# Kernel tuning notes

Measured on AMD Instinct MI355X. Metric: run time of the kernel, lower is better.

## Reference

```python
import jax, jax.numpy as jnp
import numpy as np

# Vim-S config
B, L, D, DEPTH = 16, 197, 384, 24
DI, DS, DTR = 768, 16, 24  # d_inner=2*D, d_state, dt_rank=ceil(D/16)
NUM_CLASSES = 1000
EPS = 1e-5


def setup_inputs() -> dict:
    key = jax.random.key(0)
    ks = jax.random.split(key, 12)
    f = jnp.float32
    rn = lambda k, shp, s=0.02: jax.random.normal(k, shp, f) * s
    inp = {
        'x': jax.random.normal(ks[0], (B, 3, 224, 224), f),
        'patch_w': rn(ks[1], (D, 3, 16, 16)),
        'patch_b': jnp.zeros((D,), f),
        'cls_token': rn(ks[2], (1, 1, D)),
        'pos_embed': rn(ks[3], (1, L, D)),
        'in_proj_w': rn(ks[4], (DEPTH, 2 * DI, D)),
        'conv_w': rn(ks[5], (DEPTH, DI, 1, 4), 0.1),  # depthwise causal conv, d_conv=4
        'conv_b': jnp.zeros((DEPTH, DI), f),
        'x_proj_w': rn(ks[6], (DEPTH, DTR + 2 * DS, DI)),
        'dt_proj_w': rn(ks[7], (DEPTH, DI, DTR), 0.1),
        'dt_proj_b': jnp.full((DEPTH, DI), float(np.log(np.expm1(0.01))), f),
        'A_log': jnp.log(jnp.broadcast_to(jnp.arange(1, DS + 1, dtype=f), (DEPTH, DI, DS))),
        'D_ssm': jnp.ones((DEPTH, DI), f),
        'out_proj_w': rn(ks[8], (DEPTH, D, DI)),
        'norm_w': jnp.ones((DEPTH, D), f),
        'norm_b': jnp.zeros((DEPTH, D), f),
        'normf_w': jnp.ones((D,), f),
        'normf_b': jnp.zeros((D,), f),
        'head_w': rn(ks[9], (NUM_CLASSES, D)),
        'head_b': jnp.zeros((NUM_CLASSES,), f),
    }
    return inp


def _ln(u, w, b):
    mu = u.mean(-1, keepdims=True)
    v = ((u - mu) ** 2).mean(-1, keepdims=True)
    return (u - mu) * jax.lax.rsqrt(v + EPS) * w + b


def _silu(u):
    return u * jax.nn.sigmoid(u)


def _mixer(u, Win, Wc, bc, Wx, Wdt, bdt, Alog, Dp, Wout):
    # u: [B, L, D]
    xz = jnp.einsum('bld,ed->ble', u, Win)            # [B, L, 2*DI]
    xc, z = jnp.split(xz, 2, axis=-1)
    # causal depthwise conv1d (d_conv=4): pad 3 on the left
    xt = jnp.pad(xc.transpose(0, 2, 1), ((0, 0), (0, 0), (3, 0)))
    xt = jax.lax.conv_general_dilated(xt, Wc, (1,), 'VALID',
                                      dimension_numbers=('NCH', 'OIH', 'NCH'),
                                      feature_group_count=DI)
    xc = _silu((xt + bc[None, :, None]).transpose(0, 2, 1))  # [B, L, DI]
    dbl = jnp.einsum('bld,ed->ble', xc, Wx)           # [B, L, DTR+2*DS]
    dt = jax.nn.softplus(jnp.einsum('blr,dr->bld', dbl[..., :DTR], Wdt) + bdt)
    Bm = dbl[..., DTR:DTR + DS]                       # [B, L, DS]
    Cm = dbl[..., DTR + DS:]                          # [B, L, DS]
    A = -jnp.exp(Alog)                                # [DI, DS]
    dA = jnp.exp(jnp.einsum('bld,dn->bldn', dt, A))   # [B, L, DI, DS]
    dBx = jnp.einsum('bld,bln->bldn', dt * xc, Bm)    # [B, L, DI, DS]

    def step(h, inps):
        dA_t, dBx_t, C_t = inps
        h = dA_t * h + dBx_t                          # [B, DI, DS]
        return h, jnp.einsum('bdn,bn->bd', h, C_t)

    h0 = jnp.zeros((u.shape[0], DI, DS), u.dtype)
    _, ys = jax.lax.scan(step, h0, (dA.transpose(1, 0, 2, 3),
                                    dBx.transpose(1, 0, 2, 3),
                                    Cm.transpose(1, 0, 2)))
    y = ys.transpose(1, 0, 2) + xc * Dp               # [B, L, DI]
    y = y * _silu(z)
    return jnp.einsum('ble,de->bld', y, Wout)         # [B, L, D]


def reference(x, patch_w, patch_b, cls_token, pos_embed, in_proj_w, conv_w, conv_b,
              x_proj_w, dt_proj_w, dt_proj_b, A_log, D_ssm, out_proj_w,
              norm_w, norm_b, normf_w, normf_b, head_w, head_b):
    b = x.shape[0]
    # patch embed: Conv2d(3, D, 16, stride 16)
    feat = jax.lax.conv_general_dilated(x, patch_w, (16, 16), 'VALID',
                                        dimension_numbers=('NCHW', 'OIHW', 'NCHW'))
    feat = feat + patch_b[None, :, None, None]
    tokens = feat.reshape(b, D, -1).transpose(0, 2, 1)          # [B, 196, D]
    h = jnp.concatenate([jnp.broadcast_to(cls_token, (b, 1, D)), tokens], axis=1)
    h = h + pos_embed                                           # [B, 197, D]

    def layer(carry, p):
        hid, res = carry
        Win, Wc, bc, Wx, Wdt, bdt, Alog, Dp, Wout, nw, nb = p
        res = res + hid                # (hidden + residual), first layer: residual = hidden
        hid = _mixer(_ln(res, nw, nb), Win, Wc, bc, Wx, Wdt, bdt, Alog, Dp, Wout)
        return (hid, res), None

    (hid, res), _ = jax.lax.scan(layer, (h, jnp.zeros_like(h)),
                                 (in_proj_w, conv_w, conv_b, x_proj_w, dt_proj_w,
                                  dt_proj_b, A_log, D_ssm, out_proj_w, norm_w, norm_b))
    out = _ln(res + hid, normf_w, normf_b)
    return out[:, 0] @ head_w.T + head_b                        # [B, num_classes]
```

## Files before the change

kernel.cpp:

```cpp
#include <hip/hip_runtime.h>
#include <hip/hip_bf16.h>
#include <math.h>

#define BB     16
#define LL     197
#define DD     384
#define DEPTH  24
#define DI     768
#define DSN    16
#define DTR    24
#define NC     1000
#define TT     (BB*LL)
#define NPATCH 196
#define EPSV   1e-5f

#define NCHUNK 12
#define CH     17

typedef __attribute__((ext_vector_type(8))) short short8;
typedef __attribute__((ext_vector_type(4))) short short4v;
typedef __attribute__((ext_vector_type(4))) float f32x4;

__device__ __forceinline__ short f2bf(float f) {
  union { float f; unsigned u; } v; v.f = f;
  unsigned u = v.u + 0x7fffu + ((v.u >> 16) & 1u);
  return (short)(u >> 16);
}

__device__ __forceinline__ void gload16(const short* g, const short* l) {
  __builtin_amdgcn_global_load_lds(
      (const __attribute__((address_space(1))) unsigned int*)g,
      (__attribute__((address_space(3))) unsigned int*)l, 16, 0, 0);
}

__global__ __launch_bounds__(256) void k_cvt(const float* __restrict__ src,
                                             short* __restrict__ dst, int n) {
  int i = (blockIdx.x * 256 + threadIdx.x) * 4;
  if (i + 3 < n) {
    float4 v = *(const float4*)&src[i];
    short4v o = {f2bf(v.x), f2bf(v.y), f2bf(v.z), f2bf(v.w)};
    *(short4v*)&dst[i] = o;
  } else {
    for (int j = 0; i + j < n && j < 4; j++) dst[i + j] = f2bf(src[i + j]);
  }
}

__global__ __launch_bounds__(256) void k_init(const float* __restrict__ cls,
                                              const float* __restrict__ pos,
                                              float* __restrict__ res,
                                              float* __restrict__ hid) {
  int i = blockIdx.x * 256 + threadIdx.x;
  if (i < TT * DD) res[i] = 0.f;
  if (i < BB * DD) {
    int b = i / DD, d = i % DD;
    hid[(size_t)(b * LL) * DD + d] = cls[d] + pos[d];
  }
}

__global__ __launch_bounds__(256) void k_patch(const float* __restrict__ x,
                                               const float* __restrict__ pw,
                                               const float* __restrict__ pb,
                                               const float* __restrict__ pos,
                                               float* __restrict__ hid) {
  __shared__ short sA[64 * 40];
  __shared__ short sB[64 * 40];
  const int tid = threadIdx.x;
  const int m0 = blockIdx.x * 64, n0 = blockIdx.y * 64;
  const int srow = tid >> 2;
  const int skq = (tid & 3) * 8;
  const int lane = tid & 63, w = tid >> 6;
  const int wm = (w >> 1) * 32, wn = (w & 1) * 32;
  const int fr = lane & 15;
  const int fk = (lane >> 4) * 8;
  f32x4 acc[2][2] = {};
  const int m = m0 + srow;
  const int b = m / NPATCH;
  const int p = m % NPATCH;
  const int ph = p / 14, pwi = p % 14;
  const float* Wrow = pw + (size_t)(n0 + srow) * 768 + skq;
  for (int k0 = 0; k0 < 768; k0 += 32) {
    int k = k0 + skq;
    int c = k >> 8, rr = (k >> 4) & 15, kw = k & 15;
    const float* xrow = &x[(size_t)(((b * 3 + c) * 224) + (ph * 16 + rr)) * 224 +
                           (pwi * 16 + kw)];
    float4 a0 = *(const float4*)&xrow[0];
    float4 a1 = *(const float4*)&xrow[4];
    float4 b0 = *(const float4*)&Wrow[k0];
    float4 b1 = *(const float4*)&Wrow[k0 + 4];
    short8 av = {f2bf(a0.x), f2bf(a0.y), f2bf(a0.z), f2bf(a0.w),
                 f2bf(a1.x), f2bf(a1.y), f2bf(a1.z), f2bf(a1.w)};
    short8 bv = {f2bf(b0.x), f2bf(b0.y), f2bf(b0.z), f2bf(b0.w),
                 f2bf(b1.x), f2bf(b1.y), f2bf(b1.z), f2bf(b1.w)};
    *(short8*)&sA[srow * 40 + skq] = av;
    *(short8*)&sB[srow * 40 + skq] = bv;
    __syncthreads();
    short8 af0 = *(const short8*)&sA[(wm + fr) * 40 + fk];
    short8 af1 = *(const short8*)&sA[(wm + 16 + fr) * 40 + fk];
    short8 bf0 = *(const short8*)&sB[(wn + fr) * 40 + fk];
    short8 bf1 = *(const short8*)&sB[(wn + 16 + fr) * 40 + fk];
    acc[0][0] = __builtin_amdgcn_mfma_f32_16x16x32_bf16(af0, bf0, acc[0][0], 0, 0, 0);
    acc[0][1] = __builtin_amdgcn_mfma_f32_16x16x32_bf16(af0, bf1, acc[0][1], 0, 0, 0);
    acc[1][0] = __builtin_amdgcn_mfma_f32_16x16x32_bf16(af1, bf0, acc[1][0], 0, 0, 0);
    acc[1][1] = __builtin_amdgcn_mfma_f32_16x16x32_bf16(af1, bf1, acc[1][1], 0, 0, 0);
    __syncthreads();
  }
#pragma unroll
  for (int i = 0; i < 2; i++)
#pragma unroll
    for (int j = 0; j < 2; j++)
#pragma unroll
      for (int q = 0; q < 4; q++) {
        int mm = m0 + wm + i * 16 + (lane >> 4) * 4 + q;
        int nn = n0 + wn + j * 16 + (lane & 15);
        int b2 = mm / NPATCH, pp = mm % NPATCH;
        int tok = b2 * LL + 1 + pp;
        hid[(size_t)tok * DD + nn] = acc[i][j][q] + pb[nn] + pos[(size_t)(1 + pp) * DD + nn];
      }
}

__global__ __launch_bounds__(256) void k_gemm128(const short* __restrict__ A, int lda,
                                                 const short* __restrict__ W, int ldb,
                                                 float* __restrict__ C, int ldc,
                                                 int M, int N, int K) {
  __shared__ short sA[128 * 32];
  __shared__ short sB[128 * 32];
  const int tid = threadIdx.x;
  const int lane = tid & 63, w = tid >> 6;
  const int m0 = blockIdx.x * 128, n0 = blockIdx.y * 128;
  const int wm = (w >> 1) * 64, wn = (w & 1) * 64;
  const int fr = lane & 15;
  const int fk = (lane >> 4) * 8;
  const int q0 = w * 2, q1 = w * 2 + 1;
  const int sr0 = q0 * 16 + (lane >> 2);
  const int sr1 = q1 * 16 + (lane >> 2);
  const int scol = (lane & 3) * 8;
  f32x4 acc[4][4] = {};
  const short* Ab0 = A + (size_t)(m0 + sr0) * lda + scol;
  const short* Ab1 = A + (size_t)(m0 + sr1) * lda + scol;
  const short* Bb0 = W + (size_t)(n0 + sr0) * ldb + scol;
  const short* Bb1 = W + (size_t)(n0 + sr1) * ldb + scol;
  for (int k0 = 0; k0 < K; k0 += 32) {
    gload16(Ab0 + k0, &sA[q0 * 512]);
    gload16(Ab1 + k0, &sA[q1 * 512]);
    gload16(Bb0 + k0, &sB[q0 * 512]);
    gload16(Bb1 + k0, &sB[q1 * 512]);
    __syncthreads();
    short8 af[4], bf[4];
#pragma unroll
    for (int i = 0; i < 4; i++) {
      af[i] = *(const short8*)&sA[(wm + i * 16 + fr) * 32 + fk];
      bf[i] = *(const short8*)&sB[(wn + i * 16 + fr) * 32 + fk];
    }
#pragma unroll
    for (int i = 0; i < 4; i++)
#pragma unroll
      for (int j = 0; j < 4; j++)
        acc[i][j] = __builtin_amdgcn_mfma_f32_16x16x32_bf16(af[i], bf[j], acc[i][j], 0, 0, 0);
    __syncthreads();
  }
#pragma unroll
  for (int i = 0; i < 4; i++)
#pragma unroll
    for (int j = 0; j < 4; j++)
#pragma unroll
      for (int q = 0; q < 4; q++) {
        int mm = m0 + wm + i * 16 + (lane >> 4) * 4 + q;
        int nn = n0 + wn + j * 16 + fr;
        if (mm < M) C[(size_t)mm * ldc + nn] = acc[i][j][q];
      }
}

__global__ __launch_bounds__(256) void k_gemm64(const short* __restrict__ A, int lda,
                                                const short* __restrict__ W, int ldb,
                                                float* __restrict__ C, int ldc,
                                                int M, int N, int K) {
  __shared__ short sA[64 * 32];
  __shared__ short sB[64 * 32];
  const int tid = threadIdx.x;
  const int lane = tid & 63, w = tid >> 6;
  const int m0 = blockIdx.x * 64, n0 = blockIdx.y * 64;
  const int wm = (w >> 1) * 32, wn = (w & 1) * 32;
  const int fr = lane & 15;
  const int fk = (lane >> 4) * 8;
  const int srow = w * 16 + (lane >> 2);
  const int scol = (lane & 3) * 8;
  f32x4 acc[2][2] = {};
  const short* Ab = A + (size_t)(m0 + srow) * lda + scol;
  const short* Bb = W + (size_t)(n0 + srow) * ldb + scol;
  for (int k0 = 0; k0 < K; k0 += 32) {
    gload16(Ab + k0, &sA[w * 512]);
    gload16(Bb + k0, &sB[w * 512]);
    __syncthreads();
    short8 af0 = *(const short8*)&sA[(wm + fr) * 32 + fk];
    short8 af1 = *(const short8*)&sA[(wm + 16 + fr) * 32 + fk];
    short8 bf0 = *(const short8*)&sB[(wn + fr) * 32 + fk];
    short8 bf1 = *(const short8*)&sB[(wn + 16 + fr) * 32 + fk];
    acc[0][0] = __builtin_amdgcn_mfma_f32_16x16x32_bf16(af0, bf0, acc[0][0], 0, 0, 0);
    acc[0][1] = __builtin_amdgcn_mfma_f32_16x16x32_bf16(af0, bf1, acc[0][1], 0, 0, 0);
    acc[1][0] = __builtin_amdgcn_mfma_f32_16x16x32_bf16(af1, bf0, acc[1][0], 0, 0, 0);
    acc[1][1] = __builtin_amdgcn_mfma_f32_16x16x32_bf16(af1, bf1, acc[1][1], 0, 0, 0);
    __syncthreads();
  }
#pragma unroll
  for (int i = 0; i < 2; i++)
#pragma unroll
    for (int j = 0; j < 2; j++)
#pragma unroll
      for (int q = 0; q < 4; q++) {
        int mm = m0 + wm + i * 16 + (lane >> 4) * 4 + q;
        int nn = n0 + wn + j * 16 + fr;
        if (mm < M) C[(size_t)mm * ldc + nn] = acc[i][j][q];
      }
}

__global__ __launch_bounds__(256) void k_conv(const float* __restrict__ xz,
                                              const float* __restrict__ wc,
                                              const float* __restrict__ bc,
                                              float* __restrict__ xc,
                                              short* __restrict__ xcbf) {
  int i = blockIdx.x * 256 + threadIdx.x;
  if (i >= TT * (DI / 4)) return;
  int eg = i % (DI / 4);
  int t = i / (DI / 4);
  int e = eg * 4;
  int b = t / LL, l = t % LL;
  const float* base = xz + (size_t)(b * LL) * (2 * DI) + e;
  float4 w0 = *(const float4*)&wc[(e + 0) * 4];
  float4 w1 = *(const float4*)&wc[(e + 1) * 4];
  float4 w2 = *(const float4*)&wc[(e + 2) * 4];
  float4 w3 = *(const float4*)&wc[(e + 3) * 4];
  float4 acc = *(const float4*)&bc[e];
  if (l >= 3) {
    float4 xv = *(const float4*)&base[(size_t)(l - 3) * (2 * DI)];
    acc.x += xv.x * w0.x; acc.y += xv.y * w1.x; acc.z += xv.z * w2.x; acc.w += xv.w * w3.x;
  }
  if (l >= 2) {
    float4 xv = *(const float4*)&base[(size_t)(l - 2) * (2 * DI)];
    acc.x += xv.x * w0.y; acc.y += xv.y * w1.y; acc.z += xv.z * w2.y; acc.w += xv.w * w3.y;
  }
  if (l >= 1) {
    float4 xv = *(const float4*)&base[(size_t)(l - 1) * (2 * DI)];
    acc.x += xv.x * w0.z; acc.y += xv.y * w1.z; acc.z += xv.z * w2.z; acc.w += xv.w * w3.z;
  }
  {
    float4 xv = *(const float4*)&base[(size_t)l * (2 * DI)];
    acc.x += xv.x * w0.w; acc.y += xv.y * w1.w; acc.z += xv.z * w2.w; acc.w += xv.w * w3.w;
  }
  acc.x = acc.x / (1.f + __expf(-acc.x));
  acc.y = acc.y / (1.f + __expf(-acc.y));
  acc.z = acc.z / (1.f + __expf(-acc.z));
  acc.w = acc.w / (1.f + __expf(-acc.w));
  *(float4*)&xc[(size_t)t * DI + e] = acc;
  short4v ov = {f2bf(acc.x), f2bf(acc.y), f2bf(acc.z), f2bf(acc.w)};
  *(short4v*)&xcbf[(size_t)t * DI + e] = ov;
}

__global__ __launch_bounds__(256) void k_xd(const short* __restrict__ xcbf,
                                            const short* __restrict__ wx,
                                            const short* __restrict__ wdt,
                                            const float* __restrict__ dbias,
                                            float* __restrict__ dbl,
                                            float* __restrict__ dtb) {
  __shared__ short sDT[16 * 40];
  const int tid = threadIdx.x;
  const int t0 = blockIdx.x * 16;
  const int lane = tid & 63, w = tid >> 6;
  const int fr = lane & 15;
  const int fk = (lane >> 4) * 8;
  f32x4 accx = {};
  const short* Arow = xcbf + (size_t)(t0 + fr) * DI + fk;
  const short* Wrow = wx + (size_t)(w * 16 + fr) * DI + fk;
#pragma unroll
  for (int k0 = 0; k0 < DI; k0 += 32) {
    short8 af = *(const short8*)&Arow[k0];
    short8 bf = *(const short8*)&Wrow[k0];
    accx = __builtin_amdgcn_mfma_f32_16x16x32_bf16(af, bf, accx, 0, 0, 0);
  }
  {
    int nn = w * 16 + fr;
#pragma unroll
    for (int q = 0; q < 4; q++) {
      int row = (lane >> 4) * 4 + q;
      int t = t0 + row;
      if (nn >= DTR && nn < 56) dbl[(size_t)t * 56 + nn] = accx[q];
      if (w < 2) sDT[row * 40 + nn] = (nn < DTR) ? f2bf(accx[q]) : (short)0;
    }
  }
  __syncthreads();
  short8 adt = *(const short8*)&sDT[fr * 40 + fk];
  const int g = lane >> 4;
#pragma unroll
  for (int jj = 0; jj < 12; jj++) {
    int j = w * 12 + jj;
    short8 bdt = short8{0, 0, 0, 0, 0, 0, 0, 0};
    if (g < 3) bdt = *(const short8*)&wdt[(size_t)(j * 16 + fr) * DTR + g * 8];
    f32x4 p = {};
    p = __builtin_amdgcn_mfma_f32_16x16x32_bf16(adt, bdt, p, 0, 0, 0);
    int nc = j * 16 + fr;
    float bv = dbias[nc];
#pragma unroll
    for (int q = 0; q < 4; q++) {
      int t = t0 + (lane >> 4) * 4 + q;
      float v = p[q] + bv;
      v = (v > 20.f) ? v : __logf(1.f + __expf(v));
      dtb[(size_t)t * DI + nc] = v;
    }
  }
}

__global__ __launch_bounds__(256) void k_scan1(const float* __restrict__ dt,
                                               const float* __restrict__ xc,
                                               const float* __restrict__ dbl,
                                               const float* __restrict__ Alog,
                                               float* __restrict__ Aprod,
                                               float* __restrict__ Hend) {
  const int tid = threadIdx.x;
  const int e = blockIdx.x * 128 + (tid >> 1);
  const int nh = tid & 1;
  const int b = blockIdx.y;
  const int c = blockIdx.z;
  float4 al0 = *(const float4*)&Alog[(size_t)e * DSN + nh * 8];
  float4 al1 = *(const float4*)&Alog[(size_t)e * DSN + nh * 8 + 4];
  float negA[8] = {-__expf(al0.x), -__expf(al0.y), -__expf(al0.z), -__expf(al0.w),
                   -__expf(al1.x), -__expf(al1.y), -__expf(al1.z), -__expf(al1.w)};
  float h[8] = {};
  float asum = 0.f;
  const int l0 = c * CH;
  const int l1 = (l0 + CH < LL) ? (l0 + CH) : LL;
  const size_t tbase = (size_t)b * LL;
  for (int l = l0; l < l1; l++) {
    size_t t = tbase + l;
    float dtv = dt[t * DI + e];
    float xcv = xc[t * DI + e];
    float4 B0 = *(const float4*)&dbl[t * 56 + DTR + nh * 8];
    float4 B1 = *(const float4*)&dbl[t * 56 + DTR + nh * 8 + 4];
    float dx = dtv * xcv;
    float Bv[8] = {B0.x, B0.y, B0.z, B0.w, B1.x, B1.y, B1.z, B1.w};
#pragma unroll
    for (int j = 0; j < 8; j++)
      h[j] = __expf(dtv * negA[j]) * h[j] + dx * Bv[j];
    asum += dtv;
  }
  size_t ci = (((size_t)c * BB + b) * DI + e) * DSN + nh * 8;
  *(float4*)&Aprod[ci] = float4{__expf(asum * negA[0]), __expf(asum * negA[1]),
                                __expf(asum * negA[2]), __expf(asum * negA[3])};
  *(float4*)&Aprod[ci + 4] = float4{__expf(asum * negA[4]), __expf(asum * negA[5]),
                                    __expf(asum * negA[6]), __expf(asum * negA[7])};
  *(float4*)&Hend[ci] = float4{h[0], h[1], h[2], h[3]};
  *(float4*)&Hend[ci + 4] = float4{h[4], h[5], h[6], h[7]};
}

__global__ __launch_bounds__(256) void k_scan2(const float* __restrict__ dt,
                                               const float* __restrict__ xc,
                                               const float* __restrict__ xz,
                                               const float* __restrict__ dbl,
                                               const float* __restrict__ Alog,
                                               const float* __restrict__ Dp,
                                               const float* __restrict__ Aprod,
                                               const float* __restrict__ Hend,
                                               short* __restrict__ ybf) {
  const int tid = threadIdx.x;
  const int e = blockIdx.x * 128 + (tid >> 1);
  const int nh = tid & 1;
  const int b = blockIdx.y;
  const int c = blockIdx.z;
  float4 al0 = *(const float4*)&Alog[(size_t)e * DSN + nh * 8];
  float4 al1 = *(const float4*)&Alog[(size_t)e * DSN + nh * 8 + 4];
  float negA[8] = {-__expf(al0.x), -__expf(al0.y), -__expf(al0.z), -__expf(al0.w),
                   -__expf(al1.x), -__expf(al1.y), -__expf(al1.z), -__expf(al1.w)};
  const float dpv = Dp[e];
  float h[8] = {};
  const size_t cstride = (size_t)BB * DI * DSN;
  const size_t cbase = (((size_t)b * DI + e) * DSN) + nh * 8;
  for (int cp = 0; cp < c; cp++) {
    size_t ci = (size_t)cp * cstride + cbase;
    float4 a0 = *(const float4*)&Aprod[ci];
    float4 a1 = *(const float4*)&Aprod[ci + 4];
    float4 e0 = *(const float4*)&Hend[ci];
    float4 e1 = *(const float4*)&Hend[ci + 4];
    h[0] = a0.x * h[0] + e0.x; h[1] = a0.y * h[1] + e0.y;
    h[2] = a0.z * h[2] + e0.z; h[3] = a0.w * h[3] + e0.w;
    h[4] = a1.x * h[4] + e1.x; h[5] = a1.y * h[5] + e1.y;
    h[6] = a1.z * h[6] + e1.z; h[7] = a1.w * h[7] + e1.w;
  }
  const int l0 = c * CH;
  const int l1 = (l0 + CH < LL) ? (l0 + CH) : LL;
  const size_t tbase = (size_t)b * LL;
  for (int l = l0; l < l1; l++) {
    size_t t = tbase + l;
    float dtv = dt[t * DI + e];
    float xcv = xc[t * DI + e];
    float zv = xz[t * (2 * DI) + DI + e];
    float4 B0 = *(const float4*)&dbl[t * 56 + DTR + nh * 8];
    float4 B1 = *(const float4*)&dbl[t * 56 + DTR + nh * 8 + 4];
    float4 C0 = *(const float4*)&dbl[t * 56 + DTR + DSN + nh * 8];
    float4 C1 = *(const float4*)&dbl[t * 56 + DTR + DSN + nh * 8 + 4];
    float dx = dtv * xcv;
    float Bv[8] = {B0.x, B0.y, B0.z, B0.w, B1.x, B1.y, B1.z, B1.w};
    float Cv[8] = {C0.x, C0.y, C0.z, C0.w, C1.x, C1.y, C1.z, C1.w};
    float acc = 0.f;
#pragma unroll
    for (int j = 0; j < 8; j++) {
      h[j] = __expf(dtv * negA[j]) * h[j] + dx * Bv[j];
      acc += h[j] * Cv[j];
    }
    acc += __shfl_xor(acc, 1);
    if (nh == 0) {
      float sz = zv * (1.f / (1.f + __expf(-zv)));
      ybf[t * DI + e] = f2bf((acc + xcv * dpv) * sz);
    }
  }
}

__global__ __launch_bounds__(256) void k_addln(float* __restrict__ res,
                                               const float* __restrict__ hid,
                                               short* __restrict__ u,
                                               const float* __restrict__ nw,
                                               const float* __restrict__ nb) {
  const int lane = threadIdx.x & 63;
  const int t = blockIdx.x * 4 + (threadIdx.x >> 6);
  float r[6];
  float s = 0.f, sq = 0.f;
#pragma unroll
  for (int j = 0; j < 6; j++) {
    int d = lane + j * 64;
    float v = res[(size_t)t * DD + d] + hid[(size_t)t * DD + d];
    res[(size_t)t * DD + d] = v;
    r[j] = v;
    s += v; sq += v * v;
  }
#pragma unroll
  for (int o = 32; o > 0; o >>= 1) { s += __shfl_xor(s, o); sq += __shfl_xor(sq, o); }
  float mu = s * (1.f / 384.f);
  float var = sq * (1.f / 384.f) - mu * mu;
  float rs = rsqrtf(var + EPSV);
#pragma unroll
  for (int j = 0; j < 6; j++) {
    int d = lane + j * 64;
    u[(size_t)t * DD + d] = f2bf((r[j] - mu) * rs * nw[d] + nb[d]);
  }
}

__global__ __launch_bounds__(256) void k_final(const float* __restrict__ res,
                                               const float* __restrict__ hid,
                                               const float* __restrict__ nfw,
                                               const float* __restrict__ nfb,
                                               const float* __restrict__ hw,
                                               const float* __restrict__ hb,
                                               float* __restrict__ out) {
  const int b = blockIdx.y;
  const int c0 = blockIdx.x * 125;
  const int tid = threadIdx.x;
  __shared__ float u0[DD];
  __shared__ float ls[4], lq[4];
  const size_t t0 = (size_t)b * LL * DD;
  float v0 = res[t0 + tid] + hid[t0 + tid];
  float v1 = (tid < 128) ? (res[t0 + 256 + tid] + hid[t0 + 256 + tid]) : 0.f;
  float s = v0 + v1, sq = v0 * v0 + v1 * v1;
#pragma unroll
  for (int o = 32; o > 0; o >>= 1) { s += __shfl_xor(s, o); sq += __shfl_xor(sq, o); }
  if ((tid & 63) == 0) { ls[tid >> 6] = s; lq[tid >> 6] = sq; }
  __syncthreads();
  float st = ls[0] + ls[1] + ls[2] + ls[3];
  float qt = lq[0] + lq[1] + lq[2] + lq[3];
  float mu = st * (1.f / 384.f);
  float var = qt * (1.f / 384.f) - mu * mu;
  float rs = rsqrtf(var + EPSV);
  u0[tid] = (v0 - mu) * rs * nfw[tid] + nfb[tid];
  if (tid < 128) u0[256 + tid] = (v1 - mu) * rs * nfw[256 + tid] + nfb[256 + tid];
  __syncthreads();
  int c = c0 + tid;
  if (tid < 125 && c < NC) {
    float acc = hb[c];
    const float* wrow = hw + (size_t)c * DD;
    for (int d = 0; d < DD; d += 4) {
      float4 w4 = *(const float4*)&wrow[d];
      acc += u0[d] * w4.x + u0[d + 1] * w4.y + u0[d + 2] * w4.z + u0[d + 3] * w4.w;
    }
    out[(size_t)b * NC + c] = acc;
  }
}

extern "C" void kernel_launch(void* const* d_in, const int* in_sizes, int n_in,
                              void* d_out, int out_size, void* d_ws, size_t ws_size,
                              hipStream_t stream) {
  const float* x       = (const float*)d_in[0];
  const float* patch_w = (const float*)d_in[1];
  const float* patch_b = (const float*)d_in[2];
  const float* cls     = (const float*)d_in[3];
  const float* pos     = (const float*)d_in[4];
  const float* in_proj = (const float*)d_in[5];
  const float* conv_w  = (const float*)d_in[6];
  const float* conv_b  = (const float*)d_in[7];
  const float* x_proj  = (const float*)d_in[8];
  const float* dt_w    = (const float*)d_in[9];
  const float* dt_b    = (const float*)d_in[10];
  const float* A_log   = (const float*)d_in[11];
  const float* D_ssm   = (const float*)d_in[12];
  const float* out_w   = (const float*)d_in[13];
  const float* norm_w  = (const float*)d_in[14];
  const float* norm_b  = (const float*)d_in[15];
  const float* normf_w = (const float*)d_in[16];
  const float* normf_b = (const float*)d_in[17];
  const float* head_w  = (const float*)d_in[18];
  const float* head_b  = (const float*)d_in[19];
  float* out = (float*)d_out;

  float* ws = (float*)d_ws;
  float* res = ws;  ws += (size_t)TT * DD;
  float* hid = ws;  ws += (size_t)TT * DD;
  float* u_r = ws;  ws += (size_t)TT * DD;
  float* xzb = ws;  ws += (size_t)TT * 2 * DI;
  float* xcb = ws;  ws += (size_t)TT * DI;
  float* dbl = ws;  ws += (size_t)TT * 56;
  float* dtb = ws;  ws += (size_t)TT * DI;
  float* ybf_r = ws; ws += (size_t)TT * DI / 2;
  float* xcbf_r = ws; ws += (size_t)TT * DI / 2;
  float* Aprod = ws; ws += (size_t)NCHUNK * BB * DI * DSN;
  float* Hend  = ws; ws += (size_t)NCHUNK * BB * DI * DSN;
  short* winbf  = (short*)ws; ws += (size_t)DEPTH * 2 * DI * DD / 2;
  short* woutbf = (short*)ws; ws += (size_t)DEPTH * DD * DI / 2;
  short* wxbf   = (short*)ws; ws += (size_t)DEPTH * 56 * DI / 2;
  short* wdtbf  = (short*)ws; ws += (size_t)DEPTH * DI * DTR / 2;

  short* u    = (short*)u_r;
  short* ybf  = (short*)ybf_r;
  short* xcbf = (short*)xcbf_r;

  {
    int n1 = DEPTH * 2 * DI * DD;
    k_cvt<<<(n1 / 4 + 255) / 256, 256, 0, stream>>>(in_proj, winbf, n1);
    int n2 = DEPTH * DD * DI;
    k_cvt<<<(n2 / 4 + 255) / 256, 256, 0, stream>>>(out_w, woutbf, n2);
    int n3 = DEPTH * 56 * DI;
    k_cvt<<<(n3 / 4 + 255) / 256, 256, 0, stream>>>(x_proj, wxbf, n3);
    int n4 = DEPTH * DI * DTR;
    k_cvt<<<(n4 / 4 + 255) / 256, 256, 0, stream>>>(dt_w, wdtbf, n4);
  }

  k_init<<<(TT * DD + 255) / 256, 256, 0, stream>>>(cls, pos, res, hid);
  k_patch<<<dim3(49, 6), 256, 0, stream>>>(x, patch_w, patch_b, pos, hid);

  for (int layer = 0; layer < DEPTH; layer++) {
    k_addln<<<TT / 4, 256, 0, stream>>>(res, hid, u, norm_w + layer * DD,
                                        norm_b + layer * DD);
    k_gemm128<<<dim3(25, 12), 256, 0, stream>>>(
        u, DD, winbf + (size_t)layer * 2 * DI * DD, DD, xzb, 2 * DI, TT, 2 * DI, DD);
    k_conv<<<(TT * (DI / 4) + 255) / 256, 256, 0, stream>>>(
        xzb, conv_w + layer * DI * 4, conv_b + layer * DI, xcb, xcbf);
    k_xd<<<dim3(TT / 16), 256, 0, stream>>>(
        xcbf, wxbf + (size_t)layer * 56 * DI, wdtbf + (size_t)layer * DI * DTR,
        dt_b + layer * DI, dbl, dtb);
    k_scan1<<<dim3(DI / 128, BB, NCHUNK - 1), 256, 0, stream>>>(
        dtb, xcb, dbl, A_log + (size_t)layer * DI * DSN, Aprod, Hend);
    k_scan2<<<dim3(DI / 128, BB, NCHUNK), 256, 0, stream>>>(
        dtb, xcb, xzb, dbl, A_log + (size_t)layer * DI * DSN,
        D_ssm + layer * DI, Aprod, Hend, ybf);
    k_gemm64<<<dim3(50, 6), 256, 0, stream>>>(
        ybf, DI, woutbf + (size_t)layer * DD * DI, DI, hid, DD, TT, DD, DI);
  }

  k_final<<<dim3(8, BB), 256, 0, stream>>>(res, hid, normf_w, normf_b, head_w, head_b, out);
}
```

Measured before the change: 2.594 ms.

## Fuse layernorm into in_proj GEMM, conv into x_proj, residual into out_proj

Removes the separate add+layernorm kernel. The in_proj GEMM now computes row statistics itself and normalizes fp32 residual rows into bf16 LDS tiles on the fly. The depthwise conv+SiLU is merged into the x_proj/dt kernel through shared memory, which drops the bf16 xc buffer. out_proj now accumulates directly into the residual (+=), which removes the hid buffer, and the four weight conversions are batched into one launch. This saves launches and global round-trips, but each in_proj block re-reads its residual rows for statistics, and the A-tile path loses async global-to-LDS loads.

```diff
diff --git a/kernel.cpp b/kernel.cpp
--- a/kernel.cpp
+++ b/kernel.cpp
@@ -33,9 +33,18 @@
       (__attribute__((address_space(3))) unsigned int*)l, 16, 0, 0);
 }
 
-__global__ __launch_bounds__(256) void k_cvt(const float* __restrict__ src,
-                                             short* __restrict__ dst, int n) {
-  int i = (blockIdx.x * 256 + threadIdx.x) * 4;
+__global__ __launch_bounds__(256) void k_cvt4(const float* __restrict__ s0, short* __restrict__ d0, int n0,
+                                              const float* __restrict__ s1, short* __restrict__ d1, int n1,
+                                              const float* __restrict__ s2, short* __restrict__ d2, int n2,
+                                              const float* __restrict__ s3, short* __restrict__ d3, int n3,
+                                              int b0, int b1, int b2) {
+  int blk = blockIdx.x;
+  const float* src; short* dst; int n; int lb;
+  if (blk < b0)      { src = s0; dst = d0; n = n0; lb = blk; }
+  else if (blk < b1) { src = s1; dst = d1; n = n1; lb = blk - b0; }
+  else if (blk < b2) { src = s2; dst = d2; n = n2; lb = blk - b1; }
+  else               { src = s3; dst = d3; n = n3; lb = blk - b2; }
+  int i = (lb * 256 + threadIdx.x) * 4;
   if (i + 3 < n) {
     float4 v = *(const float4*)&src[i];
     short4v o = {f2bf(v.x), f2bf(v.y), f2bf(v.z), f2bf(v.w)};
@@ -47,13 +56,11 @@
 
 __global__ __launch_bounds__(256) void k_init(const float* __restrict__ cls,
                                               const float* __restrict__ pos,
-                                              float* __restrict__ res,
-                                              float* __restrict__ hid) {
+                                              float* __restrict__ res) {
   int i = blockIdx.x * 256 + threadIdx.x;
-  if (i < TT * DD) res[i] = 0.f;
   if (i < BB * DD) {
     int b = i / DD, d = i % DD;
-    hid[(size_t)(b * LL) * DD + d] = cls[d] + pos[d];
+    res[(size_t)(b * LL) * DD + d] = cls[d] + pos[d];
   }
 }
 
@@ -61,7 +68,7 @@
                                                const float* __restrict__ pw,
                                                const float* __restrict__ pb,
                                                const float* __restrict__ pos,
-                                               float* __restrict__ hid) {
+                                               float* __restrict__ res) {
   __shared__ short sA[64 * 40];
   __shared__ short sB[64 * 40];
   const int tid = threadIdx.x;
@@ -114,19 +121,42 @@
         int nn = n0 + wn + j * 16 + (lane & 15);
         int b2 = mm / NPATCH, pp = mm % NPATCH;
         int tok = b2 * LL + 1 + pp;
-        hid[(size_t)tok * DD + nn] = acc[i][j][q] + pb[nn] + pos[(size_t)(1 + pp) * DD + nn];
+        res[(size_t)tok * DD + nn] = acc[i][j][q] + pb[nn] + pos[(size_t)(1 + pp) * DD + nn];
       }
 }
 
-__global__ __launch_bounds__(256) void k_gemm128(const short* __restrict__ A, int lda,
-                                                 const short* __restrict__ W, int ldb,
-                                                 float* __restrict__ C, int ldc,
-                                                 int M, int N, int K) {
+__global__ __launch_bounds__(256) void k_lngemm(const float* __restrict__ R,
+                                                const float* __restrict__ nw,
+                                                const float* __restrict__ nb,
+                                                const short* __restrict__ W,
+                                                float* __restrict__ C) {
   __shared__ short sA[128 * 32];
   __shared__ short sB[128 * 32];
+  __shared__ float smu[128], srs[128];
+  __shared__ float snw[DD], snb[DD];
   const int tid = threadIdx.x;
   const int lane = tid & 63, w = tid >> 6;
   const int m0 = blockIdx.x * 128, n0 = blockIdx.y * 128;
+  if (tid < 96) *(float4*)&snw[tid * 4] = *(const float4*)&nw[tid * 4];
+  else if (tid < 192) *(float4*)&snb[(tid - 96) * 4] = *(const float4*)&nb[(tid - 96) * 4];
+  {
+    int r = tid >> 1, hf = tid & 1;
+    const float* row = R + (size_t)(m0 + r) * DD + hf * 192;
+    float s = 0.f, sq = 0.f;
+#pragma unroll 4
+    for (int j = 0; j < 48; j++) {
+      float4 v = *(const float4*)&row[j * 4];
+      s += v.x + v.y + v.z + v.w;
+      sq += v.x * v.x + v.y * v.y + v.z * v.z + v.w * v.w;
+    }
+    s += __shfl_xor(s, 1); sq += __shfl_xor(sq, 1);
+    if (hf == 0) {
+      float mu = s * (1.f / 384.f);
+      float var = sq * (1.f / 384.f) - mu * mu;
+      smu[r] = mu; srs[r] = rsqrtf(var + EPSV);
+    }
+  }
+  __syncthreads();
   const int wm = (w >> 1) * 64, wn = (w & 1) * 64;
   const int fr = lane & 15;
   const int fk = (lane >> 4) * 8;
@@ -135,15 +165,41 @@
   const int sr1 = q1 * 16 + (lane >> 2);
   const int scol = (lane & 3) * 8;
   f32x4 acc[4][4] = {};
-  const short* Ab0 = A + (size_t)(m0 + sr0) * lda + scol;
-  const short* Ab1 = A + (size_t)(m0 + sr1) * lda + scol;
-  const short* Bb0 = W + (size_t)(n0 + sr0) * ldb + scol;
-  const short* Bb1 = W + (size_t)(n0 + sr1) * ldb + scol;
-  for (int k0 = 0; k0 < K; k0 += 32) {
-    gload16(Ab0 + k0, &sA[q0 * 512]);
-    gload16(Ab1 + k0, &sA[q1 * 512]);
+  const short* Bb0 = W + (size_t)(n0 + sr0) * DD + scol;
+  const short* Bb1 = W + (size_t)(n0 + sr1) * DD + scol;
+  const float* Ar0 = R + (size_t)(m0 + sr0) * DD + scol;
+  const float* Ar1 = R + (size_t)(m0 + sr1) * DD + scol;
+  const float mu0 = smu[sr0], rs0 = srs[sr0];
+  const float mu1 = smu[sr1], rs1 = srs[sr1];
+  for (int k0 = 0; k0 < DD; k0 += 32) {
     gload16(Bb0 + k0, &sB[q0 * 512]);
     gload16(Bb1 + k0, &sB[q1 * 512]);
+    float4 a0 = *(const float4*)&Ar0[k0];
+    float4 a1 = *(const float4*)&Ar0[k0 + 4];
+    float4 a2 = *(const float4*)&Ar1[k0];
+    float4 a3 = *(const float4*)&Ar1[k0 + 4];
+    float4 wa = *(const float4*)&snw[k0 + scol];
+    float4 wb = *(const float4*)&snw[k0 + scol + 4];
+    float4 ba = *(const float4*)&snb[k0 + scol];
+    float4 bb = *(const float4*)&snb[k0 + scol + 4];
+    short8 av0 = {f2bf((a0.x - mu0) * rs0 * wa.x + ba.x),
+                  f2bf((a0.y - mu0) * rs0 * wa.y + ba.y),
+                  f2bf((a0.z - mu0) * rs0 * wa.z + ba.z),
+                  f2bf((a0.w - mu0) * rs0 * wa.w + ba.w),
+                  f2bf((a1.x - mu0) * rs0 * wb.x + bb.x),
+                  f2bf((a1.y - mu0) * rs0 * wb.y + bb.y),
+                  f2bf((a1.z - mu0) * rs0 * wb.z + bb.z),
+                  f2bf((a1.w - mu0) * rs0 * wb.w + bb.w)};
+    short8 av1 = {f2bf((a2.x - mu1) * rs1 * wa.x + ba.x),
+                  f2bf((a2.y - mu1) * rs1 * wa.y + ba.y),
+                  f2bf((a2.z - mu1) * rs1 * wa.z + ba.z),
+                  f2bf((a2.w - mu1) * rs1 * wa.w + ba.w),
+                  f2bf((a3.x - mu1) * rs1 * wb.x + bb.x),
+                  f2bf((a3.y - mu1) * rs1 * wb.y + bb.y),
+                  f2bf((a3.z - mu1) * rs1 * wb.z + bb.z),
+                  f2bf((a3.w - mu1) * rs1 * wb.w + bb.w)};
+    *(short8*)&sA[q0 * 512 + lane * 8] = av0;
+    *(short8*)&sA[q1 * 512 + lane * 8] = av1;
     __syncthreads();
     short8 af[4], bf[4];
 #pragma unroll
@@ -166,7 +222,7 @@
       for (int q = 0; q < 4; q++) {
         int mm = m0 + wm + i * 16 + (lane >> 4) * 4 + q;
         int nn = n0 + wn + j * 16 + fr;
-        if (mm < M) C[(size_t)mm * ldc + nn] = acc[i][j][q];
+        if (mm < TT) C[(size_t)mm * (2 * DI) + nn] = acc[i][j][q];
       }
 }
 
@@ -209,70 +265,69 @@
       for (int q = 0; q < 4; q++) {
         int mm = m0 + wm + i * 16 + (lane >> 4) * 4 + q;
         int nn = n0 + wn + j * 16 + fr;
-        if (mm < M) C[(size_t)mm * ldc + nn] = acc[i][j][q];
+        if (mm < M) C[(size_t)mm * ldc + nn] += acc[i][j][q];
       }
 }
 
-__global__ __launch_bounds__(256) void k_conv(const float* __restrict__ xz,
+__global__ __launch_bounds__(256) void k_cxd2(const float* __restrict__ xz,
                                               const float* __restrict__ wc,
                                               const float* __restrict__ bc,
+                                              const short* __restrict__ wx,
+                                              const short* __restrict__ wdt,
+                                              const float* __restrict__ dbias,
                                               float* __restrict__ xc,
-                                              short* __restrict__ xcbf) {
-  int i = blockIdx.x * 256 + threadIdx.x;
-  if (i >= TT * (DI / 4)) return;
-  int eg = i % (DI / 4);
-  int t = i / (DI / 4);
-  int e = eg * 4;
-  int b = t / LL, l = t % LL;
-  const float* base = xz + (size_t)(b * LL) * (2 * DI) + e;
-  float4 w0 = *(const float4*)&wc[(e + 0) * 4];
-  float4 w1 = *(const float4*)&wc[(e + 1) * 4];
-  float4 w2 = *(const float4*)&wc[(e + 2) * 4];
-  float4 w3 = *(const float4*)&wc[(e + 3) * 4];
-  float4 acc = *(const float4*)&bc[e];
-  if (l >= 3) {
-    float4 xv = *(const float4*)&base[(size_t)(l - 3) * (2 * DI)];
-    acc.x += xv.x * w0.x; acc.y += xv.y * w1.x; acc.z += xv.z * w2.x; acc.w += xv.w * w3.x;
-  }
-  if (l >= 2) {
-    float4 xv = *(const float4*)&base[(size_t)(l - 2) * (2 * DI)];
-    acc.x += xv.x * w0.y; acc.y += xv.y * w1.y; acc.z += xv.z * w2.y; acc.w += xv.w * w3.y;
-  }
-  if (l >= 1) {
-    float4 xv = *(const float4*)&base[(size_t)(l - 1) * (2 * DI)];
-    acc.x += xv.x * w0.z; acc.y += xv.y * w1.z; acc.z += xv.z * w2.z; acc.w += xv.w * w3.z;
-  }
-  {
-    float4 xv = *(const float4*)&base[(size_t)l * (2 * DI)];
-    acc.x += xv.x * w0.w; acc.y += xv.y * w1.w; acc.z += xv.z * w2.w; acc.w += xv.w * w3.w;
-  }
-  acc.x = acc.x / (1.f + __expf(-acc.x));
-  acc.y = acc.y / (1.f + __expf(-acc.y));
-  acc.z = acc.z / (1.f + __expf(-acc.z));
-  acc.w = acc.w / (1.f + __expf(-acc.w));
-  *(float4*)&xc[(size_t)t * DI + e] = acc;
-  short4v ov = {f2bf(acc.x), f2bf(acc.y), f2bf(acc.z), f2bf(acc.w)};
-  *(short4v*)&xcbf[(size_t)t * DI + e] = ov;
-}
-
-__global__ __launch_bounds__(256) void k_xd(const short* __restrict__ xcbf,
-                                            const short* __restrict__ wx,
-                                            const short* __restrict__ wdt,
-                                            const float* __restrict__ dbias,
-                                            float* __restrict__ dbl,
-                                            float* __restrict__ dtb) {
+                                              float* __restrict__ dbl,
+                                              float* __restrict__ dtb) {
+  __shared__ short sXC[16 * 776];
   __shared__ short sDT[16 * 40];
   const int tid = threadIdx.x;
   const int t0 = blockIdx.x * 16;
+#pragma unroll
+  for (int it = 0; it < 12; it++) {
+    int g = tid + it * 256;
+    int tl = g / 192, eg = g % 192;
+    int e = eg * 4;
+    int t = t0 + tl;
+    int b = t / LL, l = t % LL;
+    const float* base = xz + (size_t)(b * LL) * (2 * DI) + e;
+    float4 w0 = *(const float4*)&wc[(e + 0) * 4];
+    float4 w1 = *(const float4*)&wc[(e + 1) * 4];
+    float4 w2 = *(const float4*)&wc[(e + 2) * 4];
+    float4 w3 = *(const float4*)&wc[(e + 3) * 4];
+    float4 acc = *(const float4*)&bc[e];
+    if (l >= 3) {
+      float4 xv = *(const float4*)&base[(size_t)(l - 3) * (2 * DI)];
+      acc.x += xv.x * w0.x; acc.y += xv.y * w1.x; acc.z += xv.z * w2.x; acc.w += xv.w * w3.x;
+    }
+    if (l >= 2) {
+      float4 xv = *(const float4*)&base[(size_t)(l - 2) * (2 * DI)];
+      acc.x += xv.x * w0.y; acc.y += xv.y * w1.y; acc.z += xv.z * w2.y; acc.w += xv.w * w3.y;
+    }
+    if (l >= 1) {
+      float4 xv = *(const float4*)&base[(size_t)(l - 1) * (2 * DI)];
+      acc.x += xv.x * w0.z; acc.y += xv.y * w1.z; acc.z += xv.z * w2.z; acc.w += xv.w * w3.z;
+    }
+    {
+      float4 xv = *(const float4*)&base[(size_t)l * (2 * DI)];
+      acc.x += xv.x * w0.w; acc.y += xv.y * w1.w; acc.z += xv.z * w2.w; acc.w += xv.w * w3.w;
+    }
+    acc.x = acc.x / (1.f + __expf(-acc.x));
+    acc.y = acc.y / (1.f + __expf(-acc.y));
+    acc.z = acc.z / (1.f + __expf(-acc.z));
+    acc.w = acc.w / (1.f + __expf(-acc.w));
+    *(float4*)&xc[(size_t)t * DI + e] = acc;
+    short4v ov = {f2bf(acc.x), f2bf(acc.y), f2bf(acc.z), f2bf(acc.w)};
+    *(short4v*)&sXC[tl * 776 + e] = ov;
+  }
+  __syncthreads();
   const int lane = tid & 63, w = tid >> 6;
   const int fr = lane & 15;
   const int fk = (lane >> 4) * 8;
   f32x4 accx = {};
-  const short* Arow = xcbf + (size_t)(t0 + fr) * DI + fk;
   const short* Wrow = wx + (size_t)(w * 16 + fr) * DI + fk;
 #pragma unroll
   for (int k0 = 0; k0 < DI; k0 += 32) {
-    short8 af = *(const short8*)&Arow[k0];
+    short8 af = *(const short8*)&sXC[fr * 776 + k0 + fk];
     short8 bf = *(const short8*)&Wrow[k0];
     accx = __builtin_amdgcn_mfma_f32_16x16x32_bf16(af, bf, accx, 0, 0, 0);
   }
@@ -412,37 +467,7 @@
   }
 }
 
-__global__ __launch_bounds__(256) void k_addln(float* __restrict__ res,
-                                               const float* __restrict__ hid,
-                                               short* __restrict__ u,
-                                               const float* __restrict__ nw,
-                                               const float* __restrict__ nb) {
-  const int lane = threadIdx.x & 63;
-  const int t = blockIdx.x * 4 + (threadIdx.x >> 6);
-  float r[6];
-  float s = 0.f, sq = 0.f;
-#pragma unroll
-  for (int j = 0; j < 6; j++) {
-    int d = lane + j * 64;
-    float v = res[(size_t)t * DD + d] + hid[(size_t)t * DD + d];
-    res[(size_t)t * DD + d] = v;
-    r[j] = v;
-    s += v; sq += v * v;
-  }
-#pragma unroll
-  for (int o = 32; o > 0; o >>= 1) { s += __shfl_xor(s, o); sq += __shfl_xor(sq, o); }
-  float mu = s * (1.f / 384.f);
-  float var = sq * (1.f / 384.f) - mu * mu;
-  float rs = rsqrtf(var + EPSV);
-#pragma unroll
-  for (int j = 0; j < 6; j++) {
-    int d = lane + j * 64;
-    u[(size_t)t * DD + d] = f2bf((r[j] - mu) * rs * nw[d] + nb[d]);
-  }
-}
-
 __global__ __launch_bounds__(256) void k_final(const float* __restrict__ res,
-                                               const float* __restrict__ hid,
                                                const float* __restrict__ nfw,
                                                const float* __restrict__ nfb,
                                                const float* __restrict__ hw,
@@ -454,8 +479,8 @@
   __shared__ float u0[DD];
   __shared__ float ls[4], lq[4];
   const size_t t0 = (size_t)b * LL * DD;
-  float v0 = res[t0 + tid] + hid[t0 + tid];
-  float v1 = (tid < 128) ? (res[t0 + 256 + tid] + hid[t0 + 256 + tid]) : 0.f;
+  float v0 = res[t0 + tid];
+  float v1 = (tid < 128) ? res[t0 + 256 + tid] : 0.f;
   float s = v0 + v1, sq = v0 * v0 + v1 * v1;
 #pragma unroll
   for (int o = 32; o > 0; o >>= 1) { s += __shfl_xor(s, o); sq += __shfl_xor(sq, o); }
@@ -508,14 +533,11 @@
 
   float* ws = (float*)d_ws;
   float* res = ws;  ws += (size_t)TT * DD;
-  float* hid = ws;  ws += (size_t)TT * DD;
-  float* u_r = ws;  ws += (size_t)TT * DD;
   float* xzb = ws;  ws += (size_t)TT * 2 * DI;
   float* xcb = ws;  ws += (size_t)TT * DI;
   float* dbl = ws;  ws += (size_t)TT * 56;
   float* dtb = ws;  ws += (size_t)TT * DI;
   float* ybf_r = ws; ws += (size_t)TT * DI / 2;
-  float* xcbf_r = ws; ws += (size_t)TT * DI / 2;
   float* Aprod = ws; ws += (size_t)NCHUNK * BB * DI * DSN;
   float* Hend  = ws; ws += (size_t)NCHUNK * BB * DI * DSN;
   short* winbf  = (short*)ws; ws += (size_t)DEPTH * 2 * DI * DD / 2;
@@ -523,42 +545,41 @@
   short* wxbf   = (short*)ws; ws += (size_t)DEPTH * 56 * DI / 2;
   short* wdtbf  = (short*)ws; ws += (size_t)DEPTH * DI * DTR / 2;
 
-  short* u    = (short*)u_r;
   short* ybf  = (short*)ybf_r;
-  short* xcbf = (short*)xcbf_r;
 
   {
     int n1 = DEPTH * 2 * DI * DD;
-    k_cvt<<<(n1 / 4 + 255) / 256, 256, 0, stream>>>(in_proj, winbf, n1);
     int n2 = DEPTH * DD * DI;
-    k_cvt<<<(n2 / 4 + 255) / 256, 256, 0, stream>>>(out_w, woutbf, n2);
     int n3 = DEPTH * 56 * DI;
-    k_cvt<<<(n3 / 4 + 255) / 256, 256, 0, stream>>>(x_proj, wxbf, n3);
     int n4 = DEPTH * DI * DTR;
-    k_cvt<<<(n4 / 4 + 255) / 256, 256, 0, stream>>>(dt_w, wdtbf, n4);
-  }
-
-  k_init<<<(TT * DD + 255) / 256, 256, 0, stream>>>(cls, pos, res, hid);
-  k_patch<<<dim3(49, 6), 256, 0, stream>>>(x, patch_w, patch_b, pos, hid);
+    int g1 = (n1 / 4 + 255) / 256;
+    int g2 = (n2 / 4 + 255) / 256;
+    int g3 = (n3 / 4 + 255) / 256;
+    int g4 = (n4 / 4 + 255) / 256;
+    k_cvt4<<<g1 + g2 + g3 + g4, 256, 0, stream>>>(
+        in_proj, winbf, n1, out_w, woutbf, n2, x_proj, wxbf, n3, dt_w, wdtbf, n4,
+        g1, g1 + g2, g1 + g2 + g3);
+  }
+
+  k_init<<<(BB * DD + 255) / 256, 256, 0, stream>>>(cls, pos, res);
+  k_patch<<<dim3(49, 6), 256, 0, stream>>>(x, patch_w, patch_b, pos, res);
 
   for (int layer = 0; layer < DEPTH; layer++) {
-    k_addln<<<TT / 4, 256, 0, stream>>>(res, hid, u, norm_w + layer * DD,
-                                        norm_b + layer * DD);
-    k_gemm128<<<dim3(25, 12), 256, 0, stream>>>(
-        u, DD, winbf + (size_t)layer * 2 * DI * DD, DD, xzb, 2 * DI, TT, 2 * DI, DD);
-    k_conv<<<(TT * (DI / 4) + 255) / 256, 256, 0, stream>>>(
-        xzb, conv_w + layer * DI * 4, conv_b + layer * DI, xcb, xcbf);
-    k_xd<<<dim3(TT / 16), 256, 0, stream>>>(
-        xcbf, wxbf + (size_t)layer * 56 * DI, wdtbf + (size_t)layer * DI * DTR,
-        dt_b + layer * DI, dbl, dtb);
+    k_lngemm<<<dim3(25, 12), 256, 0, stream>>>(
+        res, norm_w + layer * DD, norm_b + layer * DD,
+        winbf + (size_t)layer * 2 * DI * DD, xzb);
+    k_cxd2<<<dim3(TT / 16), 256, 0, stream>>>(
+        xzb, conv_w + layer * DI * 4, conv_b + layer * DI,
+        wxbf + (size_t)layer * 56 * DI, wdtbf + (size_t)layer * DI * DTR,
+        dt_b + layer * DI, xcb, dbl, dtb);
     k_scan1<<<dim3(DI / 128, BB, NCHUNK - 1), 256, 0, stream>>>(
         dtb, xcb, dbl, A_log + (size_t)layer * DI * DSN, Aprod, Hend);
     k_scan2<<<dim3(DI / 128, BB, NCHUNK), 256, 0, stream>>>(
         dtb, xcb, xzb, dbl, A_log + (size_t)layer * DI * DSN,
         D_ssm + layer * DI, Aprod, Hend, ybf);
     k_gemm64<<<dim3(50, 6), 256, 0, stream>>>(
-        ybf, DI, woutbf + (size_t)layer * DD * DI, DI, hid, DD, TT, DD, DI);
-  }
-
-  k_final<<<dim3(8, BB), 256, 0, stream>>>(res, hid, normf_w, normf_b, head_w, head_b, out);
-}
+        ybf, DI, woutbf + (size_t)layer * DD * DI, DI, res, DD, TT, DD, DI);
+  }
+
+  k_final<<<dim3(8, BB), 256, 0, stream>>>(res, normf_w, normf_b, head_w, head_b, out);
+}
```

Measured after the change: 2.936 ms. 1.13x slower.
